# Kernel tuning notes

Hardware: AMD Instinct MI355X
Metric: run time of the kernel (lower is better)

The kernel has to match this reference:

```python
import jax, jax.numpy as jnp
import numpy as np

E = 1_000_000   # total edges across batch
B = 1024        # n_batch (graphs)
IN = 128
OUT = 128


def setup_inputs() -> dict:
    key = jax.random.key(0)
    ks = jax.random.split(key, 8)
    x1 = jax.random.normal(ks[0], (E, IN), dtype=jnp.float32)
    # cumulative slice boundaries: [0, sorted interior cuts, E]
    inner = jnp.sort(jax.random.randint(ks[1], (B - 1,), 0, E))
    edge_slices = jnp.concatenate([jnp.zeros((1,), jnp.int32),
                                   inner.astype(jnp.int32),
                                   jnp.full((1,), E, jnp.int32)])
    s1 = 1.0 / np.sqrt(IN)
    s2 = 1.0 / np.sqrt(OUT)
    W1 = jax.random.uniform(ks[2], (IN, OUT), jnp.float32, -s1, s1)
    b1 = jax.random.uniform(ks[3], (OUT,), jnp.float32, -s1, s1)
    W2 = jax.random.uniform(ks[4], (OUT, OUT), jnp.float32, -s2, s2)
    b2 = jax.random.uniform(ks[5], (OUT,), jnp.float32, -s2, s2)
    W3 = jax.random.uniform(ks[6], (OUT, OUT), jnp.float32, -s2, s2)
    b3 = jax.random.uniform(ks[7], (OUT,), jnp.float32, -s2, s2)
    return {"x1": x1, "edge_slices": edge_slices,
            "W1": W1, "b1": b1, "W2": W2, "b2": b2, "W3": W3, "b3": b3}


def reference(x1, edge_slices, W1, b1, W2, b2, W3, b3):
    n_edges = x1.shape[0]
    n_batch = edge_slices.shape[0] - 1
    # internal MLP: Linear -> ReLU -> Linear
    h = jax.nn.relu(x1 @ W1 + b1) @ W2 + b2  # [E, OUT]
    # segment id of edge i: index of slice containing i (replaces repeat_interleave)
    seg = jnp.searchsorted(edge_slices[1:], jnp.arange(n_edges), side='right')
    sums = jax.ops.segment_sum(h, seg, num_segments=n_batch)        # [B, OUT]
    counts = (edge_slices[1:] - edge_slices[:-1]).astype(h.dtype)   # [B]
    mean = sums / jnp.maximum(counts, 1.0)[:, None]  # empty segments -> 0 (matches scatter-mean)
    # external MLP: single Linear
    return mean @ W3 + b3
```

## Files before the change

### kernel.cpp

```cpp
#include <hip/hip_runtime.h>
#include <hip/hip_bf16.h>

typedef __attribute__((ext_vector_type(8))) short short8;
typedef __attribute__((ext_vector_type(4))) float floatx4;
typedef unsigned short u16;
typedef unsigned int u32;

#define D 128
#define TM 64
#define NT 4
#define CHUNK (TM*NT)
#define LDSX 136

static __device__ __forceinline__ u16 f2bf(float f) {
  union { float f; u32 u; } v; v.f = f;
  u32 r = v.u + 0x7fffu + ((v.u >> 16) & 1u);
  return (u16)(r >> 16);
}

__global__ void prep_kernel(const float* __restrict__ W1, u16* __restrict__ W1T,
                            float* __restrict__ S, int nS)
{
  int t = blockIdx.x * blockDim.x + threadIdx.x;
  if (t < D * D) {
    int k = t >> 7;
    int n = t & (D - 1);
    W1T[n * D + k] = f2bf(W1[t]);
  }
  if (t < nS) S[t] = 0.f;
}

__global__ __launch_bounds__(256, 3)
void fused_mlp_segsum(const float* __restrict__ x1,
                      const int* __restrict__ slices,
                      const u16* __restrict__ W1T,
                      const float* __restrict__ b1,
                      float* __restrict__ S,
                      int E, int B)
{
  __shared__ __align__(16) u16 xt[2][TM * LDSX];

  const int tid  = threadIdx.x;
  const int wv   = tid >> 6;
  const int lane = tid & 63;
  const int quad = lane >> 4;
  const int l16  = lane & 15;

  const int chunkStart = blockIdx.x * CHUNK;
  const int chunkEnd   = min(chunkStart + CHUNK, E);
  const int ntiles     = (chunkEnd - chunkStart + TM - 1) / TM;

  short8 bf[2][4];
  #pragma unroll
  for (int c = 0; c < 2; ++c)
    #pragma unroll
    for (int kk = 0; kk < 4; ++kk)
      bf[c][kk] = *(const short8*)(W1T + ((2 * wv + c) * 16 + l16) * D + kk * 32 + quad * 8);

  float bias[2] = { b1[wv * 32 + l16], b1[wv * 32 + 16 + l16] };

  int l = 0, r = B + 1;
  while (l < r) { int m = (l + r) >> 1; if (slices[m] <= chunkStart) l = m + 1; else r = m; }
  int cur = l - 1;
  float racc0 = 0.f, racc1 = 0.f;

  {
    #pragma unroll
    for (int i = 0; i < 8; ++i) {
      int f = tid + i * 256;
      int row = chunkStart + (f >> 5);
      int c = (f & 31) * 4;
      int rr = min(row, E - 1);
      float4 v = *(const float4*)(x1 + (size_t)rr * D + c);
      if (row >= E) { v.x = 0.f; v.y = 0.f; v.z = 0.f; v.w = 0.f; }
      uint2 pk;
      pk.x = (u32)f2bf(v.x) | ((u32)f2bf(v.y) << 16);
      pk.y = (u32)f2bf(v.z) | ((u32)f2bf(v.w) << 16);
      *(uint2*)(&xt[0][(f >> 5) * LDSX + c]) = pk;
    }
  }
  __syncthreads();

  for (int t = 0; t < ntiles; ++t) {
    const int base = chunkStart + t * TM;

    float4 ld[8];
    const bool havePf = (t + 1 < ntiles);
    if (havePf) {
      int nb = base + TM;
      #pragma unroll
      for (int i = 0; i < 8; ++i) {
        int f = tid + i * 256;
        int row = nb + (f >> 5);
        int rr = min(row, E - 1);
        ld[i] = *(const float4*)(x1 + (size_t)rr * D + (f & 31) * 4);
        if (row >= E) { ld[i].x = 0.f; ld[i].y = 0.f; ld[i].z = 0.f; ld[i].w = 0.f; }
      }
    }

    const u16* xb = xt[t & 1];
    floatx4 acc[4][2];
    #pragma unroll
    for (int rt = 0; rt < 4; ++rt)
      #pragma unroll
      for (int c = 0; c < 2; ++c)
        acc[rt][c] = (floatx4){0.f, 0.f, 0.f, 0.f};

    #pragma unroll
    for (int kk = 0; kk < 4; ++kk) {
      #pragma unroll
      for (int rt = 0; rt < 4; ++rt) {
        short8 a = *(const short8*)(xb + (rt * 16 + l16) * LDSX + kk * 32 + quad * 8);
        acc[rt][0] = __builtin_amdgcn_mfma_f32_16x16x32_bf16(a, bf[0][kk], acc[rt][0], 0, 0, 0);
        acc[rt][1] = __builtin_amdgcn_mfma_f32_16x16x32_bf16(a, bf[1][kk], acc[rt][1], 0, 0, 0);
      }
    }

    #pragma unroll
    for (int rt = 0; rt < 4; ++rt)
      #pragma unroll
      for (int c = 0; c < 2; ++c)
        #pragma unroll
        for (int i = 0; i < 4; ++i)
          acc[rt][c][i] = fmaxf(acc[rt][c][i] + bias[c], 0.f);

    const int tileHi = min(base + TM, chunkEnd);

    auto segAdd = [&](int loR, int hiR) {
      #pragma unroll
      for (int rt = 0; rt < 4; ++rt)
        #pragma unroll
        for (int i = 0; i < 4; ++i) {
          int rowOff = rt * 16 + quad * 4 + i;
          bool in = (rowOff >= loR) && (rowOff < hiR);
          racc0 += in ? acc[rt][0][i] : 0.f;
          racc1 += in ? acc[rt][1][i] : 0.f;
        }
    };
    auto flushSeg = [&](int s) {
      float t0 = racc0, t1 = racc1;
      t0 += __shfl_xor(t0, 16); t0 += __shfl_xor(t0, 32);
      t1 += __shfl_xor(t1, 16); t1 += __shfl_xor(t1, 32);
      if (quad == 0) {
        atomicAdd(&S[s * D + wv * 32 + l16], t0);
        atomicAdd(&S[s * D + wv * 32 + 16 + l16], t1);
      }
    };

    while (cur < B) {
      int segEnd = slices[cur + 1];
      if (segEnd > tileHi) break;
      int lo = max(slices[cur], base);
      if (segEnd > lo) segAdd(lo - base, segEnd - base);
      flushSeg(cur);
      racc0 = 0.f; racc1 = 0.f;
      ++cur;
    }
    if (cur < B) {
      int lo = max(slices[cur], base);
      if (lo < tileHi) {
        if (lo == base && tileHi == base + TM) {
          #pragma unroll
          for (int rt = 0; rt < 4; ++rt)
            #pragma unroll
            for (int i = 0; i < 4; ++i) { racc0 += acc[rt][0][i]; racc1 += acc[rt][1][i]; }
        } else {
          segAdd(lo - base, tileHi - base);
        }
      }
    }

    if (havePf) {
      u16* dst = xt[(t + 1) & 1];
      #pragma unroll
      for (int i = 0; i < 8; ++i) {
        int f = tid + i * 256;
        uint2 pk;
        pk.x = (u32)f2bf(ld[i].x) | ((u32)f2bf(ld[i].y) << 16);
        pk.y = (u32)f2bf(ld[i].z) | ((u32)f2bf(ld[i].w) << 16);
        *(uint2*)(&dst[(f >> 5) * LDSX + (f & 31) * 4]) = pk;
      }
    }
    __syncthreads();
  }

  if (cur < B && slices[cur] < chunkEnd) {
    float t0 = racc0, t1 = racc1;
    t0 += __shfl_xor(t0, 16); t0 += __shfl_xor(t0, 32);
    t1 += __shfl_xor(t1, 16); t1 += __shfl_xor(t1, 32);
    if (quad == 0) {
      atomicAdd(&S[cur * D + wv * 32 + l16], t0);
      atomicAdd(&S[cur * D + wv * 32 + 16 + l16], t1);
    }
  }
}

__global__ __launch_bounds__(128)
void finish_mlp(const float* __restrict__ S, const int* __restrict__ slices,
                const float* __restrict__ W2, const float* __restrict__ b2,
                const float* __restrict__ W3, const float* __restrict__ b3,
                float* __restrict__ out, int B)
{
  __shared__ float v0[D];
  __shared__ float v1[D];
  int s = blockIdx.x;
  int j = threadIdx.x;
  int c0 = slices[s], c1 = slices[s + 1];
  int cnt = c1 - c0;
  if (cnt <= 0) { out[s * D + j] = b3[j]; return; }
  v0[j] = S[s * D + j] * (1.f / (float)cnt);
  __syncthreads();
  float a = b2[j];
  #pragma unroll 8
  for (int k = 0; k < D; ++k) a = fmaf(v0[k], W2[k * D + j], a);
  v1[j] = a;
  __syncthreads();
  float o = b3[j];
  #pragma unroll 8
  for (int k = 0; k < D; ++k) o = fmaf(v1[k], W3[k * D + j], o);
  out[s * D + j] = o;
}

extern "C" void kernel_launch(void* const* d_in, const int* in_sizes, int n_in,
                              void* d_out, int out_size, void* d_ws, size_t ws_size,
                              hipStream_t stream) {
  const float* x1     = (const float*)d_in[0];
  const int*   slices = (const int*)d_in[1];
  const float* W1     = (const float*)d_in[2];
  const float* b1     = (const float*)d_in[3];
  const float* W2     = (const float*)d_in[4];
  const float* b2     = (const float*)d_in[5];
  const float* W3     = (const float*)d_in[6];
  const float* b3     = (const float*)d_in[7];
  float* out = (float*)d_out;

  const int E = in_sizes[0] / D;
  const int B = in_sizes[1] - 1;

  float* S   = (float*)d_ws;
  u16*   W1T = (u16*)((char*)d_ws + (size_t)B * D * 4);

  int nS = B * D;
  prep_kernel<<<(nS + 255) / 256, 256, 0, stream>>>(W1, W1T, S, nS);

  int nblk = (E + CHUNK - 1) / CHUNK;
  fused_mlp_segsum<<<nblk, 256, 0, stream>>>(x1, slices, W1T, b1, S, E, B);

  finish_mlp<<<B, D, 0, stream>>>(S, slices, W2, b2, W3, b3, out, B);
}
```

Baseline: 675.2 us.

## Load x rows directly into MFMA registers, dropping LDS staging and barriers

The fused kernel no longer stages each 64-row tile through double-buffered LDS. Each wave now loads its own 16-row groups from global memory straight into the MFMA A-operand layout and converts to bf16 with a perm-based packer. Loads are double-buffered in registers one group ahead. This removes LDS traffic and __syncthreads. In exchange, all four waves redundantly load the same x rows, since each wave computes a different 32-column slice, and segment bookkeeping now runs per 16-row group. The new bf16 conversion rounds half away from zero instead of round-to-nearest-even, and out-of-range rows are clamped to the last valid row rather than zeroed.

```diff
diff --git a/kernel.cpp b/kernel.cpp
--- a/kernel.cpp
+++ b/kernel.cpp
@@ -7,15 +7,19 @@
 typedef unsigned int u32;
 
 #define D 128
-#define TM 64
-#define NT 4
-#define CHUNK (TM*NT)
-#define LDSX 136
+#define CHUNK 256
+#define NG 16
 
 static __device__ __forceinline__ u16 f2bf(float f) {
   union { float f; u32 u; } v; v.f = f;
   u32 r = v.u + 0x7fffu + ((v.u >> 16) & 1u);
   return (u16)(r >> 16);
+}
+
+static __device__ __forceinline__ u32 pk2bf(float lo, float hi) {
+  union { float f; u32 u; } a, b;
+  a.f = lo; b.f = hi;
+  return __builtin_amdgcn_perm(b.u + 0x8000u, a.u + 0x8000u, 0x07060302);
 }
 
 __global__ void prep_kernel(const float* __restrict__ W1, u16* __restrict__ W1T,
@@ -38,8 +42,6 @@
                       float* __restrict__ S,
                       int E, int B)
 {
-  __shared__ __align__(16) u16 xt[2][TM * LDSX];
-
   const int tid  = threadIdx.x;
   const int wv   = tid >> 6;
   const int lane = tid & 63;
@@ -48,7 +50,7 @@
 
   const int chunkStart = blockIdx.x * CHUNK;
   const int chunkEnd   = min(chunkStart + CHUNK, E);
-  const int ntiles     = (chunkEnd - chunkStart + TM - 1) / TM;
+  const int ngroups    = (chunkEnd - chunkStart + 15) >> 4;
 
   short8 bf[2][4];
   #pragma unroll
@@ -57,142 +59,104 @@
     for (int kk = 0; kk < 4; ++kk)
       bf[c][kk] = *(const short8*)(W1T + ((2 * wv + c) * 16 + l16) * D + kk * 32 + quad * 8);
 
-  float bias[2] = { b1[wv * 32 + l16], b1[wv * 32 + 16 + l16] };
+  const float bias0 = b1[wv * 32 + l16];
+  const float bias1 = b1[wv * 32 + 16 + l16];
 
   int l = 0, r = B + 1;
   while (l < r) { int m = (l + r) >> 1; if (slices[m] <= chunkStart) l = m + 1; else r = m; }
   int cur = l - 1;
   float racc0 = 0.f, racc1 = 0.f;
 
-  {
-    #pragma unroll
-    for (int i = 0; i < 8; ++i) {
-      int f = tid + i * 256;
-      int row = chunkStart + (f >> 5);
-      int c = (f & 31) * 4;
-      int rr = min(row, E - 1);
-      float4 v = *(const float4*)(x1 + (size_t)rr * D + c);
-      if (row >= E) { v.x = 0.f; v.y = 0.f; v.z = 0.f; v.w = 0.f; }
-      uint2 pk;
-      pk.x = (u32)f2bf(v.x) | ((u32)f2bf(v.y) << 16);
-      pk.y = (u32)f2bf(v.z) | ((u32)f2bf(v.w) << 16);
-      *(uint2*)(&xt[0][(f >> 5) * LDSX + c]) = pk;
-    }
-  }
-  __syncthreads();
-
-  for (int t = 0; t < ntiles; ++t) {
-    const int base = chunkStart + t * TM;
-
-    float4 ld[8];
-    const bool havePf = (t + 1 < ntiles);
-    if (havePf) {
-      int nb = base + TM;
-      #pragma unroll
-      for (int i = 0; i < 8; ++i) {
-        int f = tid + i * 256;
-        int row = nb + (f >> 5);
-        int rr = min(row, E - 1);
-        ld[i] = *(const float4*)(x1 + (size_t)rr * D + (f & 31) * 4);
-        if (row >= E) { ld[i].x = 0.f; ld[i].y = 0.f; ld[i].z = 0.f; ld[i].w = 0.f; }
-      }
-    }
-
-    const u16* xb = xt[t & 1];
-    floatx4 acc[4][2];
-    #pragma unroll
-    for (int rt = 0; rt < 4; ++rt)
-      #pragma unroll
-      for (int c = 0; c < 2; ++c)
-        acc[rt][c] = (floatx4){0.f, 0.f, 0.f, 0.f};
-
+  auto loadGroup = [&](int g, float4 f0[4], float4 f1[4]) {
+    int row = chunkStart + g * 16 + l16;
+    const float* rp = x1 + (size_t)min(row, E - 1) * D + quad * 8;
     #pragma unroll
     for (int kk = 0; kk < 4; ++kk) {
-      #pragma unroll
-      for (int rt = 0; rt < 4; ++rt) {
-        short8 a = *(const short8*)(xb + (rt * 16 + l16) * LDSX + kk * 32 + quad * 8);
-        acc[rt][0] = __builtin_amdgcn_mfma_f32_16x16x32_bf16(a, bf[0][kk], acc[rt][0], 0, 0, 0);
-        acc[rt][1] = __builtin_amdgcn_mfma_f32_16x16x32_bf16(a, bf[1][kk], acc[rt][1], 0, 0, 0);
-      }
-    }
-
-    #pragma unroll
-    for (int rt = 0; rt < 4; ++rt)
-      #pragma unroll
-      for (int c = 0; c < 2; ++c)
-        #pragma unroll
-        for (int i = 0; i < 4; ++i)
-          acc[rt][c][i] = fmaxf(acc[rt][c][i] + bias[c], 0.f);
-
-    const int tileHi = min(base + TM, chunkEnd);
-
-    auto segAdd = [&](int loR, int hiR) {
-      #pragma unroll
-      for (int rt = 0; rt < 4; ++rt)
-        #pragma unroll
-        for (int i = 0; i < 4; ++i) {
-          int rowOff = rt * 16 + quad * 4 + i;
-          bool in = (rowOff >= loR) && (rowOff < hiR);
-          racc0 += in ? acc[rt][0][i] : 0.f;
-          racc1 += in ? acc[rt][1][i] : 0.f;
-        }
-    };
-    auto flushSeg = [&](int s) {
-      float t0 = racc0, t1 = racc1;
-      t0 += __shfl_xor(t0, 16); t0 += __shfl_xor(t0, 32);
-      t1 += __shfl_xor(t1, 16); t1 += __shfl_xor(t1, 32);
-      if (quad == 0) {
-        atomicAdd(&S[s * D + wv * 32 + l16], t0);
-        atomicAdd(&S[s * D + wv * 32 + 16 + l16], t1);
-      }
-    };
-
-    while (cur < B) {
-      int segEnd = slices[cur + 1];
-      if (segEnd > tileHi) break;
-      int lo = max(slices[cur], base);
-      if (segEnd > lo) segAdd(lo - base, segEnd - base);
-      flushSeg(cur);
-      racc0 = 0.f; racc1 = 0.f;
-      ++cur;
-    }
-    if (cur < B) {
-      int lo = max(slices[cur], base);
-      if (lo < tileHi) {
-        if (lo == base && tileHi == base + TM) {
-          #pragma unroll
-          for (int rt = 0; rt < 4; ++rt)
-            #pragma unroll
-            for (int i = 0; i < 4; ++i) { racc0 += acc[rt][0][i]; racc1 += acc[rt][1][i]; }
-        } else {
-          segAdd(lo - base, tileHi - base);
-        }
-      }
-    }
-
-    if (havePf) {
-      u16* dst = xt[(t + 1) & 1];
-      #pragma unroll
-      for (int i = 0; i < 8; ++i) {
-        int f = tid + i * 256;
-        uint2 pk;
-        pk.x = (u32)f2bf(ld[i].x) | ((u32)f2bf(ld[i].y) << 16);
-        pk.y = (u32)f2bf(ld[i].z) | ((u32)f2bf(ld[i].w) << 16);
-        *(uint2*)(&dst[(f >> 5) * LDSX + (f & 31) * 4]) = pk;
-      }
-    }
-    __syncthreads();
-  }
-
-  if (cur < B && slices[cur] < chunkEnd) {
+      f0[kk] = *(const float4*)(rp + kk * 32);
+      f1[kk] = *(const float4*)(rp + kk * 32 + 4);
+    }
+  };
+
+  auto flushSeg = [&](int s) {
     float t0 = racc0, t1 = racc1;
     t0 += __shfl_xor(t0, 16); t0 += __shfl_xor(t0, 32);
     t1 += __shfl_xor(t1, 16); t1 += __shfl_xor(t1, 32);
     if (quad == 0) {
-      atomicAdd(&S[cur * D + wv * 32 + l16], t0);
-      atomicAdd(&S[cur * D + wv * 32 + 16 + l16], t1);
+      atomicAdd(&S[s * D + wv * 32 + l16], t0);
+      atomicAdd(&S[s * D + wv * 32 + 16 + l16], t1);
+    }
+    racc0 = 0.f; racc1 = 0.f;
+  };
+
+  auto compute = [&](int g, const float4 f0[4], const float4 f1[4]) {
+    floatx4 a0 = (floatx4){0.f, 0.f, 0.f, 0.f};
+    floatx4 a1 = (floatx4){0.f, 0.f, 0.f, 0.f};
+    #pragma unroll
+    for (int kk = 0; kk < 4; ++kk) {
+      union { short8 s; u32 u[4]; } A;
+      A.u[0] = pk2bf(f0[kk].x, f0[kk].y);
+      A.u[1] = pk2bf(f0[kk].z, f0[kk].w);
+      A.u[2] = pk2bf(f1[kk].x, f1[kk].y);
+      A.u[3] = pk2bf(f1[kk].z, f1[kk].w);
+      a0 = __builtin_amdgcn_mfma_f32_16x16x32_bf16(A.s, bf[0][kk], a0, 0, 0, 0);
+      a1 = __builtin_amdgcn_mfma_f32_16x16x32_bf16(A.s, bf[1][kk], a1, 0, 0, 0);
+    }
+    #pragma unroll
+    for (int i = 0; i < 4; ++i) {
+      a0[i] = fmaxf(a0[i] + bias0, 0.f);
+      a1[i] = fmaxf(a1[i] + bias1, 0.f);
+    }
+    const int base = chunkStart + g * 16;
+    const int hi16 = min(base + 16, chunkEnd);
+    while (cur < B) {
+      int segEnd = slices[cur + 1];
+      if (segEnd > hi16) break;
+      int loR = max(slices[cur], base) - base;
+      int hiR = segEnd - base;
+      if (hiR > loR) {
+        #pragma unroll
+        for (int i = 0; i < 4; ++i) {
+          int rowOff = quad * 4 + i;
+          bool in = (rowOff >= loR) && (rowOff < hiR);
+          racc0 += in ? a0[i] : 0.f;
+          racc1 += in ? a1[i] : 0.f;
+        }
+      }
+      flushSeg(cur);
+      ++cur;
+    }
+    if (cur < B) {
+      int lo = max(slices[cur], base);
+      if (lo < hi16) {
+        if (lo == base && hi16 == base + 16) {
+          #pragma unroll
+          for (int i = 0; i < 4; ++i) { racc0 += a0[i]; racc1 += a1[i]; }
+        } else {
+          int loR = lo - base, hiR = hi16 - base;
+          #pragma unroll
+          for (int i = 0; i < 4; ++i) {
+            int rowOff = quad * 4 + i;
+            bool in = (rowOff >= loR) && (rowOff < hiR);
+            racc0 += in ? a0[i] : 0.f;
+            racc1 += in ? a1[i] : 0.f;
+          }
+        }
+      }
+    }
+  };
+
+  float4 c0[4], c1[4], n0[4], n1[4];
+  loadGroup(0, c0, c1);
+  for (int g = 0; g < ngroups; g += 2) {
+    if (g + 1 < ngroups) loadGroup(g + 1, n0, n1);
+    compute(g, c0, c1);
+    if (g + 1 < ngroups) {
+      if (g + 2 < ngroups) loadGroup(g + 2, c0, c1);
+      compute(g + 1, n0, n1);
     }
   }
+
+  if (cur < B && slices[cur] < chunkEnd) flushSeg(cur);
 }
 
 __global__ __launch_bounds__(128)
```

Result: slower. 777.9 us (+15.2%).
